# Kernel optimization log

Hardware: AMD Instinct MI355X
Metric: run time of the kernel (lower is better)

## Reference

```python
import jax, jax.numpy as jnp
import numpy as np
from jax import lax

NUM_ITER = 10
SMOOTH = 1.0
CL_WEIGHT = 0.5


def _min_pool(x, wh, ww):
    # torch: -max_pool2d(-x) pads with -inf -> min-pool with +inf boundary
    return lax.reduce_window(x, jnp.inf, lax.min,
                             (1, 1, wh, ww), (1, 1, 1, 1),
                             [(0, 0), (0, 0), (wh // 2, wh // 2), (ww // 2, ww // 2)])


def _max_pool(x, wh, ww):
    return lax.reduce_window(x, -jnp.inf, lax.max,
                             (1, 1, wh, ww), (1, 1, 1, 1),
                             [(0, 0), (0, 0), (wh // 2, wh // 2), (ww // 2, ww // 2)])


def soft_erode(img):
    return jnp.minimum(_min_pool(img, 3, 1), _min_pool(img, 1, 3))


def soft_dilate(img):
    return _max_pool(img, 3, 3)


def soft_open(img):
    return soft_dilate(soft_erode(img))


def soft_skeleton(img, num_iter=NUM_ITER):
    # img: (B,1,H,W)
    skel = jax.nn.relu(img - soft_open(img))

    def body(i, carry):
        img_e, skel = carry
        img_e = soft_erode(img_e)
        delta = jax.nn.relu(img_e - soft_open(img_e))
        skel = skel + jax.nn.relu(delta - skel * delta)
        return (img_e, skel)

    _, skel = lax.fori_loop(0, num_iter, body, (img, skel))
    return skel


def soft_dice(pred, target, smooth=SMOOTH):
    inter = jnp.sum(pred * target)
    return (2.0 * inter + smooth) / (jnp.sum(pred) + jnp.sum(target) + smooth)


def setup_inputs() -> dict:
    key = jax.random.key(0)
    k1, k2 = jax.random.split(key)
    pred = jax.random.normal(k1, (8, 1, 1024, 1024), dtype=jnp.float32)
    target = jax.random.randint(k2, (8, 1, 1024, 1024), 0, 2, dtype=jnp.int32)
    return {"pred": pred, "target": target}


def reference(pred, target):
    pred_prob = jax.nn.sigmoid(pred)          # (B,1,H,W)
    target_f = target.astype(pred_prob.dtype)

    skel_pred = soft_skeleton(pred_prob)
    skel_target = soft_skeleton(target_f)

    tprec = (jnp.sum(skel_pred * target_f) + SMOOTH) / (jnp.sum(skel_pred) + SMOOTH)
    tsens = (jnp.sum(skel_target * pred_prob) + SMOOTH) / (jnp.sum(skel_target) + SMOOTH)
    cl_dice = 2.0 * tprec * tsens / (tprec + tsens + 1e-7)

    dice = soft_dice(pred_prob, target_f)
    combined = (1.0 - CL_WEIGHT) * dice + CL_WEIGHT * cl_dice
    loss = 1.0 - combined
    return loss
```

## Files before the change

### kernel.cpp

```cpp
#include <hip/hip_runtime.h>
#include <math.h>

#define IMG  1024
#define TILE 64
#define HALO 12
#define SPP  52
#define NPRED (88*SPP)
#define SEN2 0x40004000u

typedef _Float16 h2 __attribute__((ext_vector_type(2)));
union UH { unsigned u; h2 h; };
__device__ __forceinline__ h2 u2h(unsigned u){ UH x; x.u=u; return x.h; }
__device__ __forceinline__ unsigned h2u(h2 h){ UH x; x.h=h; return x.u; }
__device__ __forceinline__ h2 pmin(h2 a, h2 b){ return __builtin_elementwise_min(a,b); }
__device__ __forceinline__ h2 pmax(h2 a, h2 b){ return __builtin_elementwise_max(a,b); }
__device__ __forceinline__ h2 funnel(h2 hi_src, h2 lo_src){
  return u2h((h2u(lo_src)>>16) | (h2u(hi_src)<<16));
}
__device__ __forceinline__ float sigmoidf(float x){ return 1.0f/(1.0f+__expf(-x)); }
__device__ __forceinline__ h2 unsent(h2 x, h2 onev, h2 zerov){
  h2 t = pmax(x-onev, zerov); return x - t - t;
}
__device__ __forceinline__ unsigned extract8(unsigned w0, unsigned w1, unsigned w2, int bp){
  unsigned long long lo = (unsigned long long)w0 | ((unsigned long long)w1<<32);
  unsigned long long hi = (unsigned long long)w1 | ((unsigned long long)w2<<32);
  unsigned a = (unsigned)(lo >> bp);
  unsigned b = (unsigned)(hi >> (bp & 31));
  return ((bp < 32) ? a : b) & 0xFFu;
}

__device__ __forceinline__ void erode2p(const unsigned* A, unsigned* B, int o){
  uint4 up = *(const uint4*)&A[o - SPP];
  uint4 c0 = *(const uint4*)&A[o];
  uint4 c1 = *(const uint4*)&A[o + SPP];
  uint4 dn = *(const uint4*)&A[o + 2*SPP];
  unsigned l0 = A[o-1], l1 = A[o+SPP-1], rr0 = A[o+4], rr1 = A[o+SPP+4];
  h2 a0=u2h(c0.x),a1=u2h(c0.y),a2=u2h(c0.z),a3=u2h(c0.w);
  h2 b0=u2h(c1.x),b1=u2h(c1.y),b2=u2h(c1.z),b3=u2h(c1.w);
  h2 va0=pmin(u2h(up.x),b0), va1=pmin(u2h(up.y),b1), va2=pmin(u2h(up.z),b2), va3=pmin(u2h(up.w),b3);
  h2 vb0=pmin(a0,u2h(dn.x)), vb1=pmin(a1,u2h(dn.y)), vb2=pmin(a2,u2h(dn.z)), vb3=pmin(a3,u2h(dn.w));
  h2 f0=funnel(a0,u2h(l0)), f1=funnel(a1,a0), f2=funnel(a2,a1), f3=funnel(a3,a2), f4=funnel(u2h(rr0),a3);
  h2 g0=funnel(b0,u2h(l1)), g1=funnel(b1,b0), g2=funnel(b2,b1), g3=funnel(b3,b2), g4=funnel(u2h(rr1),b3);
  uint4 e0,e1;
  e0.x=h2u(pmin(pmin(f0,f1),pmin(va0,a0)));
  e0.y=h2u(pmin(pmin(f1,f2),pmin(va1,a1)));
  e0.z=h2u(pmin(pmin(f2,f3),pmin(va2,a2)));
  e0.w=h2u(pmin(pmin(f3,f4),pmin(va3,a3)));
  e1.x=h2u(pmin(pmin(g0,g1),pmin(vb0,b0)));
  e1.y=h2u(pmin(pmin(g1,g2),pmin(vb1,b1)));
  e1.z=h2u(pmin(pmin(g2,g3),pmin(vb2,b2)));
  e1.w=h2u(pmin(pmin(g3,g4),pmin(vb3,b3)));
  *(uint4*)&B[o]      = e0;
  *(uint4*)&B[o+SPP]  = e1;
}

template<bool BND>
__device__ void pipeline(const float* __restrict__ pred, const int* __restrict__ targ,
                         long base, int gr0, int gc0, int tid,
                         unsigned* PA, unsigned* PB, unsigned* TAi, unsigned* TBi,
                         unsigned* sK,
                         h2 val[8], h2 skel[8], unsigned &tbits, unsigned &skbits) {
  if (!BND) {
    #pragma unroll
    for (int k=0;k<4;++k){
      int u = tid + (k<<8);
      if (u < 968) {
        int r = u/11, q = u - r*11;
        long g = base + (long)(gr0+r)*IMG + gc0 + (q<<3);
        float4 pa = *(const float4*)(pred+g);
        float4 pb = *(const float4*)(pred+g+4);
        h2 w0 = {(_Float16)sigmoidf(pa.x), (_Float16)sigmoidf(pa.y)};
        h2 w1 = {(_Float16)sigmoidf(pa.z), (_Float16)sigmoidf(pa.w)};
        h2 w2 = {(_Float16)sigmoidf(pb.x), (_Float16)sigmoidf(pb.y)};
        h2 w3 = {(_Float16)sigmoidf(pb.z), (_Float16)sigmoidf(pb.w)};
        int o = r*SPP + 2 + (q<<2);
        uint2 d0; d0.x=h2u(w0); d0.y=h2u(w1);
        uint2 d1; d1.x=h2u(w2); d1.y=h2u(w3);
        *(uint2*)&PA[o]   = d0;
        *(uint2*)&PA[o+2] = d1;
      }
    }
    #pragma unroll
    for (int k=0;k<2;++k){
      int u = tid + (k<<8);
      if (u < 264) {
        int r = u/3, w = u - r*3;
        long g = base + (long)(gr0+r)*IMG + gc0 + (w<<5);
        unsigned bits = 0;
        #pragma unroll
        for (int i=0;i<8;++i){
          if (w < 2 || i < 6) {
            int4 tv = *(const int4*)(targ + g + (i<<2));
            unsigned nib = (unsigned)(tv.x!=0) | ((unsigned)(tv.y!=0)<<1)
                         | ((unsigned)(tv.z!=0)<<2) | ((unsigned)(tv.w!=0)<<3);
            bits |= nib << (i<<2);
          }
        }
        if (w==2) bits |= 0xFF000000u;
        TAi[u] = bits;
      }
    }
  } else {
    for (int i=tid; i<88*44; i+=256){
      int r = i/44, wd = i - r*44;
      int gr = gr0 + r;
      bool rok = (unsigned)gr < (unsigned)IMG;
      int gca = gc0 + (wd<<1), gcb = gca + 1;
      _Float16 va = (_Float16)2.0f, vb = (_Float16)2.0f;
      if (rok && (unsigned)gca < (unsigned)IMG) va = (_Float16)sigmoidf(pred[base + (long)gr*IMG + gca]);
      if (rok && (unsigned)gcb < (unsigned)IMG) vb = (_Float16)sigmoidf(pred[base + (long)gr*IMG + gcb]);
      h2 w; w.x = va; w.y = vb;
      PA[r*SPP + 2 + wd] = h2u(w);
    }
    for (int u=tid; u<264; u+=256){
      int r = u/3, w = u - r*3;
      int gr = gr0 + r;
      bool rok = (unsigned)gr < (unsigned)IMG;
      unsigned bits = 0;
      for (int b=0;b<32;++b){
        int c = (w<<5) + b;
        unsigned bit = 1;
        if (c < 88) {
          int gc = gc0 + c;
          if (rok && (unsigned)gc < (unsigned)IMG) bit = (unsigned)(targ[base+(long)gr*IMG+gc] != 0);
        }
        bits |= bit << b;
      }
      TAi[u] = bits;
    }
  }
  __syncthreads();

  unsigned cm0=~0u, cm1=~0u, cm2=0x00FFFFFFu;
  bool colO = false;
  if (BND) {
    int lo = (-gc0 > 0) ? -gc0 : 0;
    int hi = (IMG - gc0 < 88) ? (IMG - gc0) : 88;
    colO = (lo > 0) || (hi < 88);
    unsigned m[3];
    #pragma unroll
    for (int w=0; w<3; ++w){
      int l = lo - (w<<5); if (l<0) l=0;
      int h = hi - (w<<5); if (h>32) h=32;
      unsigned mm = 0;
      if (h > l) {
        unsigned top = (h>=32)? ~0u : ((1u<<h)-1u);
        unsigned bot = (l<=0)? 0u : ((1u<<l)-1u);
        mm = top & ~bot;
      }
      m[w]=mm;
    }
    cm0=m[0]; cm1=m[1]; cm2=m[2] & 0x00FFFFFF;
  }

  int eo0, eo1, eo2 = 0;
  { int u=tid;     int s=u/12, q=u-s*12; eo0 = (1+(s<<1))*SPP + (q<<2); }
  { int u=tid+256; int s=u/12, q=u-s*12; eo1 = (1+(s<<1))*SPP + (q<<2); }
  const bool eex = (tid < 4);
  if (eex) { int u=tid+512; int s=u/12, q=u-s*12; eo2 = (1+(s<<1))*SPP + (q<<2); }
  const int to  = 3 + tid;
  const int twd = tid - (tid/3)*3;
  const bool tex = (tid < 2);
  const int to2  = 3 + 256 + tid;
  const int twd2 = (256+tid) - ((256+tid)/3)*3;

  const int qc = tid & 7;
  const int rg = tid >> 3;
  const int r0 = HALO + (rg<<1);
  const int wq = 8 + (qc<<2);
  const int bp = 12 + (qc<<3);

  h2 ep[8];
  {
    uint4 a0 = *(const uint4*)&PA[r0*SPP + wq];
    uint4 a1 = *(const uint4*)&PA[(r0+1)*SPP + wq];
    ep[0]=u2h(a0.x); ep[1]=u2h(a0.y); ep[2]=u2h(a0.z); ep[3]=u2h(a0.w);
    ep[4]=u2h(a1.x); ep[5]=u2h(a1.y); ep[6]=u2h(a1.z); ep[7]=u2h(a1.w);
    #pragma unroll
    for (int i=0;i<8;++i){ val[i]=ep[i]; skel[i]=(h2)(_Float16)0.0f; }
  }
  {
    int oa = r0*3, ob = (r0+1)*3;
    tbits = extract8(TAi[oa],TAi[oa+1],TAi[oa+2],bp)
          | (extract8(TAi[ob],TAi[ob+1],TAi[ob+2],bp) << 8);
  }
  unsigned tp0=0,tp1=0,tp2=0, sk0=0,sk1=0,sk2=0;
  const bool td = (tid < 64);
  const int tro = (12 + tid)*3;
  if (td) { tp0=TAi[tro]; tp1=TAi[tro+1]; tp2=TAi[tro+2]; }

  const h2 onev  = {(_Float16)1.0f,(_Float16)1.0f};
  const h2 zerov = {(_Float16)0.0f,(_Float16)0.0f};
  unsigned *A=PA, *B=PB, *Ta=TAi, *Tb=TBi;

  for (int j=0;j<11;++j){
    erode2p(A,B,eo0);
    erode2p(A,B,eo1);
    if (eex) erode2p(A,B,eo2);
    {
      unsigned own=Ta[to], up=Ta[to-3], dn=Ta[to+3];
      unsigned le = (twd>0)? Ta[to-1] : ~0u;
      unsigned ri = (twd<2)? Ta[to+1] : ~0u;
      unsigned h = own & ((own>>1)|(ri<<31)) & ((own<<1)|(le>>31));
      Tb[to] = h & up & dn;
    }
    if (tex) {
      unsigned own=Ta[to2], up=Ta[to2-3], dn=Ta[to2+3];
      unsigned le = (twd2>0)? Ta[to2-1] : ~0u;
      unsigned ri = (twd2<2)? Ta[to2+1] : ~0u;
      unsigned h = own & ((own>>1)|(ri<<31)) & ((own<<1)|(le>>31));
      Tb[to2] = h & up & dn;
    }
    __syncthreads();

    if (BND) {
      if (gr0 < 0) {
        for (int i=tid;i<12*44;i+=256){ int r=i/44; B[r*SPP+2+(i-r*44)] = SEN2; }
        if (tid < 36) Tb[tid] = ~0u;
      }
      if (gr0 + 88 > IMG) {
        for (int i=tid;i<12*44;i+=256){ int r=i/44; B[(76+r)*SPP+2+(i-r*44)] = SEN2; }
        if (tid < 36) Tb[228+tid] = ~0u;
      }
      if (colO) {
        if (gc0 < 0)
          for (int i=tid;i<88*6;i+=256){ int r=i/6; B[r*SPP+2+(i-r*6)] = SEN2; }
        if (gc0 + 88 > IMG)
          for (int i=tid;i<88*6;i+=256){ int r=i/6; B[r*SPP+40+(i-r*6)] = SEN2; }
        for (int i=tid;i<264;i+=256){
          int r=i/3, w=i-r*3;
          unsigned nm = (w==0)?~cm0:((w==1)?~cm1:~cm2);
          Tb[i] |= nm;
        }
      }
      __syncthreads();
    }

    h2 H[4][4];
    uint4 cap0, cap1;
    #pragma unroll
    for (int k=0;k<4;++k){
      int ro = (r0-1+k)*SPP + wq;
      uint4 c = *(const uint4*)&B[ro];
      h2 lw = u2h(B[ro-1]);
      h2 rw = u2h(B[ro+4]);
      if (k==1) cap0 = c;
      if (k==2) cap1 = c;
      h2 a0=u2h(c.x),a1=u2h(c.y),a2=u2h(c.z),a3=u2h(c.w);
      if (BND){
        a0=unsent(a0,onev,zerov); a1=unsent(a1,onev,zerov);
        a2=unsent(a2,onev,zerov); a3=unsent(a3,onev,zerov);
        lw=unsent(lw,onev,zerov); rw=unsent(rw,onev,zerov);
      }
      h2 f0=funnel(a0,lw), f1=funnel(a1,a0), f2=funnel(a2,a1), f3=funnel(a3,a2), f4=funnel(rw,a3);
      H[k][0]=pmax(pmax(f0,f1),a0);
      H[k][1]=pmax(pmax(f1,f2),a1);
      H[k][2]=pmax(pmax(f2,f3),a2);
      H[k][3]=pmax(pmax(f3,f4),a3);
    }
    #pragma unroll
    for (int i=0;i<4;++i){
      h2 m0 = pmax(pmax(H[0][i],H[1][i]),H[2][i]);
      h2 m1 = pmax(pmax(H[1][i],H[2][i]),H[3][i]);
      h2 d0 = pmax(ep[i]-m0, zerov);
      h2 d1 = pmax(ep[4+i]-m1, zerov);
      h2 x0 = d0 - skel[i]*d0;
      h2 x1 = d1 - skel[4+i]*d1;
      skel[i]   = skel[i]   + pmax(x0, zerov);
      skel[4+i] = skel[4+i] + pmax(x1, zerov);
    }
    ep[0]=u2h(cap0.x); ep[1]=u2h(cap0.y); ep[2]=u2h(cap0.z); ep[3]=u2h(cap0.w);
    ep[4]=u2h(cap1.x); ep[5]=u2h(cap1.y); ep[6]=u2h(cap1.z); ep[7]=u2h(cap1.w);

    if (td) {
      unsigned o0=Tb[tro], o1=Tb[tro+1], o2=Tb[tro+2];
      unsigned u0=Tb[tro-3], u1=Tb[tro-2], u2=Tb[tro-1];
      unsigned n0=Tb[tro+3], n1=Tb[tro+4], n2=Tb[tro+5];
      unsigned v0,v1,v2;
      if (BND){
        unsigned mu = ((unsigned)(gr0 + 11 + tid) < (unsigned)IMG) ? ~0u : 0u;
        unsigned md = ((unsigned)(gr0 + 13 + tid) < (unsigned)IMG) ? ~0u : 0u;
        v0 = ((u0&mu)|o0|(n0&md)) & cm0;
        v1 = ((u1&mu)|o1|(n1&md)) & cm1;
        v2 = ((u2&mu)|o2|(n2&md)) & cm2;
      } else {
        v0 = u0|o0|n0; v1 = u1|o1|n1; v2 = u2|o2|n2;
      }
      unsigned d0 = v0 | (v0<<1) | (v0>>1) | (v1<<31);
      unsigned d1 = v1 | (v1<<1) | (v0>>31) | (v1>>1) | (v2<<31);
      unsigned d2 = v2 | (v2<<1) | (v1>>31) | (v2>>1);
      sk0 |= tp0 & ~d0;
      sk1 |= tp1 & ~d1;
      sk2 |= tp2 & ~d2;
      tp0 = o0; tp1 = o1; tp2 = o2;
    }
    unsigned* t1 = A;  A = B;  B = t1;
    unsigned* t2 = Ta; Ta = Tb; Tb = t2;
  }

  if (td){ sK[3*tid] = sk0; sK[3*tid+1] = sk1; sK[3*tid+2] = sk2; }
  __syncthreads();
  {
    int o = (r0-12)*3;
    skbits = extract8(sK[o],sK[o+1],sK[o+2],bp)
           | (extract8(sK[o+3],sK[o+4],sK[o+5],bp) << 8);
  }
}

__global__ __launch_bounds__(256,4)
void cl_dice_main(const float* __restrict__ pred, const int* __restrict__ targ,
                  float* __restrict__ ws) {
  __shared__ alignas(16) unsigned sPA[NPRED];
  __shared__ alignas(16) unsigned sPB[NPRED];
  __shared__ unsigned sTA[264], sTB[264], sK[192];
  const int tid = threadIdx.x;
  const int gr0 = blockIdx.y * TILE - HALO;
  const int gc0 = blockIdx.x * TILE - HALO;
  const long base = (long)blockIdx.z * (long)(IMG * IMG);

  h2 val[8], skel[8]; unsigned tbits, skbits;
  const bool bnd = (blockIdx.x == 0) | (blockIdx.x == gridDim.x - 1) |
                   (blockIdx.y == 0) | (blockIdx.y == gridDim.y - 1);
  if (!bnd) pipeline<false>(pred, targ, base, gr0, gc0, tid, sPA, sPB, sTA, sTB, sK, val, skel, tbits, skbits);
  else      pipeline<true >(pred, targ, base, gr0, gc0, tid, sPA, sPB, sTA, sTB, sK, val, skel, tbits, skbits);

  float s[7] = {0,0,0,0,0,0,0};
  #pragma unroll
  for (int k=0;k<8;++k){
    int bb = ((k>>2)<<3) + ((k&3)<<1);
    float p0=(float)val[k].x,  p1=(float)val[k].y;
    float a0=(float)skel[k].x, a1=(float)skel[k].y;
    float t0=(float)((tbits>>bb)&1u),    t1=(float)((tbits>>(bb+1))&1u);
    float b0=(float)((skbits>>bb)&1u),   b1=(float)((skbits>>(bb+1))&1u);
    s[0]+=a0+a1;        s[1]+=a0*t0+a1*t1;
    s[2]+=b0+b1;        s[3]+=b0*p0+b1*p1;
    s[4]+=p0*t0+p1*t1;  s[5]+=p0+p1;  s[6]+=t0+t1;
  }

  float* red = (float*)sPA;
  #pragma unroll
  for (int k=0;k<7;++k){
    float v = s[k];
    v += __shfl_down(v,32); v += __shfl_down(v,16); v += __shfl_down(v,8);
    v += __shfl_down(v,4);  v += __shfl_down(v,2);  v += __shfl_down(v,1);
    if ((tid & 63) == 0) red[(tid>>6)*8 + k] = v;
  }
  __syncthreads();
  if (tid < 7) {
    float v = red[tid] + red[8+tid] + red[16+tid] + red[24+tid];
    int blk = (blockIdx.z * gridDim.y + blockIdx.y) * gridDim.x + blockIdx.x;
    ws[blk*8 + tid] = v;
  }
}

__global__ __launch_bounds__(256)
void cl_dice_finalize(const float* __restrict__ ws, float* __restrict__ out, int nblk) {
  __shared__ float red[4][8];
  int tid = threadIdx.x;
  float acc[7] = {0,0,0,0,0,0,0};
  for (int i=tid; i<nblk; i+=256) {
    #pragma unroll
    for (int k=0;k<7;++k) acc[k] += ws[i*8 + k];
  }
  #pragma unroll
  for (int k=0;k<7;++k){
    float v = acc[k];
    v += __shfl_down(v,32); v += __shfl_down(v,16); v += __shfl_down(v,8);
    v += __shfl_down(v,4);  v += __shfl_down(v,2);  v += __shfl_down(v,1);
    if ((tid & 63) == 0) red[tid>>6][k] = v;
  }
  __syncthreads();
  if (tid == 0) {
    float t0[7];
    #pragma unroll
    for (int k=0;k<7;++k) t0[k] = red[0][k] + red[1][k] + red[2][k] + red[3][k];
    float sum_sp = t0[0], sum_spt = t0[1], sum_st = t0[2], sum_stp = t0[3];
    float inter  = t0[4], sum_p   = t0[5], sum_t  = t0[6];
    float tprec = (sum_spt + 1.0f) / (sum_sp + 1.0f);
    float tsens = (sum_stp + 1.0f) / (sum_st + 1.0f);
    float cl    = 2.0f * tprec * tsens / (tprec + tsens + 1e-7f);
    float dice  = (2.0f * inter + 1.0f) / (sum_p + sum_t + 1.0f);
    out[0] = 1.0f - 0.5f * (dice + cl);
  }
}

extern "C" void kernel_launch(void* const* d_in, const int* in_sizes, int n_in,
                              void* d_out, int out_size, void* d_ws, size_t ws_size,
                              hipStream_t stream) {
  const float* pred = (const float*)d_in[0];
  const int*   targ = (const int*)d_in[1];
  float* ws  = (float*)d_ws;
  float* out = (float*)d_out;

  const int B = in_sizes[0] / (IMG * IMG);
  dim3 grid(IMG / TILE, IMG / TILE, B);
  cl_dice_main<<<grid, 256, 0, stream>>>(pred, targ, ws);

  const int nblk = (IMG / TILE) * (IMG / TILE) * B;
  cl_dice_finalize<<<1, 256, 0, stream>>>(ws, out, nblk);
}
```

Before: 249.6 us.

## Erode in place with single shared buffer and register-blocked row strips

Replaces the ping-pong shared buffers with one buffer (plus sentinel border rows) that is eroded in place. Each thread computes a strip of 5 row-pairs in registers, a barrier follows, and then the results are written back. The erode work also shrinks by iteration as the valid region narrows. Halving LDS use allows raising launch bounds to 8 blocks per CU, which targets occupancy and reuses vertical neighbours across rows, at the cost of an extra barrier per iteration and more register pressure.

Measured after the change: 321.3 us. 1.29x slower.

```diff
diff --git a/kernel.cpp b/kernel.cpp
--- a/kernel.cpp
+++ b/kernel.cpp
@@ -5,7 +5,7 @@
 #define TILE 64
 #define HALO 12
 #define SPP  52
-#define NPRED (88*SPP)
+#define NPRED (90*SPP)
 #define SEN2 0x40004000u
 
 typedef _Float16 h2 __attribute__((ext_vector_type(2)));
@@ -29,42 +29,25 @@
   return ((bp < 32) ? a : b) & 0xFFu;
 }
 
-__device__ __forceinline__ void erode2p(const unsigned* A, unsigned* B, int o){
-  uint4 up = *(const uint4*)&A[o - SPP];
-  uint4 c0 = *(const uint4*)&A[o];
-  uint4 c1 = *(const uint4*)&A[o + SPP];
-  uint4 dn = *(const uint4*)&A[o + 2*SPP];
-  unsigned l0 = A[o-1], l1 = A[o+SPP-1], rr0 = A[o+4], rr1 = A[o+SPP+4];
-  h2 a0=u2h(c0.x),a1=u2h(c0.y),a2=u2h(c0.z),a3=u2h(c0.w);
-  h2 b0=u2h(c1.x),b1=u2h(c1.y),b2=u2h(c1.z),b3=u2h(c1.w);
-  h2 va0=pmin(u2h(up.x),b0), va1=pmin(u2h(up.y),b1), va2=pmin(u2h(up.z),b2), va3=pmin(u2h(up.w),b3);
-  h2 vb0=pmin(a0,u2h(dn.x)), vb1=pmin(a1,u2h(dn.y)), vb2=pmin(a2,u2h(dn.z)), vb3=pmin(a3,u2h(dn.w));
-  h2 f0=funnel(a0,u2h(l0)), f1=funnel(a1,a0), f2=funnel(a2,a1), f3=funnel(a3,a2), f4=funnel(u2h(rr0),a3);
-  h2 g0=funnel(b0,u2h(l1)), g1=funnel(b1,b0), g2=funnel(b2,b1), g3=funnel(b3,b2), g4=funnel(u2h(rr1),b3);
-  uint4 e0,e1;
-  e0.x=h2u(pmin(pmin(f0,f1),pmin(va0,a0)));
-  e0.y=h2u(pmin(pmin(f1,f2),pmin(va1,a1)));
-  e0.z=h2u(pmin(pmin(f2,f3),pmin(va2,a2)));
-  e0.w=h2u(pmin(pmin(f3,f4),pmin(va3,a3)));
-  e1.x=h2u(pmin(pmin(g0,g1),pmin(vb0,b0)));
-  e1.y=h2u(pmin(pmin(g1,g2),pmin(vb1,b1)));
-  e1.z=h2u(pmin(pmin(g2,g3),pmin(vb2,b2)));
-  e1.w=h2u(pmin(pmin(g3,g4),pmin(vb3,b3)));
-  *(uint4*)&B[o]      = e0;
-  *(uint4*)&B[o+SPP]  = e1;
-}
-
 template<bool BND>
 __device__ void pipeline(const float* __restrict__ pred, const int* __restrict__ targ,
                          long base, int gr0, int gc0, int tid,
-                         unsigned* PA, unsigned* PB, unsigned* TAi, unsigned* TBi,
-                         unsigned* sK,
+                         unsigned* P, unsigned* Ta,
                          h2 val[8], h2 skel[8], unsigned &tbits, unsigned &skbits) {
+  for (int i = tid; i < 104; i += 256) {
+    int r = (i < 52) ? 0 : 89, c = (i < 52) ? i : i - 52;
+    P[r*SPP + c] = SEN2;
+  }
+  for (int i = tid; i < 704; i += 256) {
+    int r = 1 + (i >> 3), w = i & 7;
+    w = (w < 2) ? w : 44 + w;
+    P[r*SPP + w] = SEN2;
+  }
   if (!BND) {
     #pragma unroll
     for (int k=0;k<4;++k){
       int u = tid + (k<<8);
-      if (u < 968) {
+      if (u < 968){
         int r = u/11, q = u - r*11;
         long g = base + (long)(gr0+r)*IMG + gc0 + (q<<3);
         float4 pa = *(const float4*)(pred+g);
@@ -73,17 +56,17 @@
         h2 w1 = {(_Float16)sigmoidf(pa.z), (_Float16)sigmoidf(pa.w)};
         h2 w2 = {(_Float16)sigmoidf(pb.x), (_Float16)sigmoidf(pb.y)};
         h2 w3 = {(_Float16)sigmoidf(pb.z), (_Float16)sigmoidf(pb.w)};
-        int o = r*SPP + 2 + (q<<2);
+        int o = (1+r)*SPP + 2 + (q<<2);
         uint2 d0; d0.x=h2u(w0); d0.y=h2u(w1);
         uint2 d1; d1.x=h2u(w2); d1.y=h2u(w3);
-        *(uint2*)&PA[o]   = d0;
-        *(uint2*)&PA[o+2] = d1;
+        *(uint2*)&P[o]   = d0;
+        *(uint2*)&P[o+2] = d1;
       }
     }
     #pragma unroll
     for (int k=0;k<2;++k){
       int u = tid + (k<<8);
-      if (u < 264) {
+      if (u < 264){
         int r = u/3, w = u - r*3;
         long g = base + (long)(gr0+r)*IMG + gc0 + (w<<5);
         unsigned bits = 0;
@@ -97,7 +80,7 @@
           }
         }
         if (w==2) bits |= 0xFF000000u;
-        TAi[u] = bits;
+        Ta[u] = bits;
       }
     }
   } else {
@@ -110,7 +93,7 @@
       if (rok && (unsigned)gca < (unsigned)IMG) va = (_Float16)sigmoidf(pred[base + (long)gr*IMG + gca]);
       if (rok && (unsigned)gcb < (unsigned)IMG) vb = (_Float16)sigmoidf(pred[base + (long)gr*IMG + gcb]);
       h2 w; w.x = va; w.y = vb;
-      PA[r*SPP + 2 + wd] = h2u(w);
+      P[(1+r)*SPP + 2 + wd] = h2u(w);
     }
     for (int u=tid; u<264; u+=256){
       int r = u/3, w = u - r*3;
@@ -126,7 +109,7 @@
         }
         bits |= bit << b;
       }
-      TAi[u] = bits;
+      Ta[u] = bits;
     }
   }
   __syncthreads();
@@ -153,15 +136,14 @@
     cm0=m[0]; cm1=m[1]; cm2=m[2] & 0x00FFFFFF;
   }
 
-  int eo0, eo1, eo2 = 0;
-  { int u=tid;     int s=u/12, q=u-s*12; eo0 = (1+(s<<1))*SPP + (q<<2); }
-  { int u=tid+256; int s=u/12, q=u-s*12; eo1 = (1+(s<<1))*SPP + (q<<2); }
-  const bool eex = (tid < 4);
-  if (eex) { int u=tid+512; int s=u/12, q=u-s*12; eo2 = (1+(s<<1))*SPP + (q<<2); }
-  const int to  = 3 + tid;
+  const bool eact0 = (tid < 216);
+  const int es = tid / 12, eq = tid - es*12;
+  const int s5 = es * 5;
+  const int ew = eq << 2;
+  const int to = 3 + tid;
   const int twd = tid - (tid/3)*3;
   const bool tex = (tid < 2);
-  const int to2  = 3 + 256 + tid;
+  const int to2 = 259 + tid;
   const int twd2 = (256+tid) - ((256+tid)/3)*3;
 
   const int qc = tid & 7;
@@ -172,8 +154,8 @@
 
   h2 ep[8];
   {
-    uint4 a0 = *(const uint4*)&PA[r0*SPP + wq];
-    uint4 a1 = *(const uint4*)&PA[(r0+1)*SPP + wq];
+    uint4 a0 = *(const uint4*)&P[(r0+1)*SPP + wq];
+    uint4 a1 = *(const uint4*)&P[(r0+2)*SPP + wq];
     ep[0]=u2h(a0.x); ep[1]=u2h(a0.y); ep[2]=u2h(a0.z); ep[3]=u2h(a0.w);
     ep[4]=u2h(a1.x); ep[5]=u2h(a1.y); ep[6]=u2h(a1.z); ep[7]=u2h(a1.w);
     #pragma unroll
@@ -181,56 +163,94 @@
   }
   {
     int oa = r0*3, ob = (r0+1)*3;
-    tbits = extract8(TAi[oa],TAi[oa+1],TAi[oa+2],bp)
-          | (extract8(TAi[ob],TAi[ob+1],TAi[ob+2],bp) << 8);
+    tbits = extract8(Ta[oa],Ta[oa+1],Ta[oa+2],bp)
+          | (extract8(Ta[ob],Ta[ob+1],Ta[ob+2],bp) << 8);
   }
   unsigned tp0=0,tp1=0,tp2=0, sk0=0,sk1=0,sk2=0;
   const bool td = (tid < 64);
   const int tro = (12 + tid)*3;
-  if (td) { tp0=TAi[tro]; tp1=TAi[tro+1]; tp2=TAi[tro+2]; }
+  if (td) { tp0=Ta[tro]; tp1=Ta[tro+1]; tp2=Ta[tro+2]; }
 
   const h2 onev  = {(_Float16)1.0f,(_Float16)1.0f};
   const h2 zerov = {(_Float16)0.0f,(_Float16)0.0f};
-  unsigned *A=PA, *B=PB, *Ta=TAi, *Tb=TBi;
 
   for (int j=0;j<11;++j){
-    erode2p(A,B,eo0);
-    erode2p(A,B,eo1);
-    if (eex) erode2p(A,B,eo2);
+    uint4 e[5];
+    const bool act = eact0 && (s5+4 >= j+1) && (s5 <= 86-j);
+    if (act){
+      uint4 rw[7];
+      #pragma unroll
+      for (int t=0;t<7;++t){
+        int pr = s5 - 1 + t; pr = (pr > 88) ? 88 : pr;
+        rw[t] = *(const uint4*)&P[(pr+1)*SPP + ew];
+      }
+      h2 lw[5], rv[5];
+      #pragma unroll
+      for (int t=0;t<5;++t){
+        int pr = s5 + t; pr = (pr > 88) ? 88 : pr;
+        lw[t] = u2h(P[(pr+1)*SPP + ew - 1]);
+        rv[t] = u2h(P[(pr+1)*SPP + ew + 4]);
+      }
+      #pragma unroll
+      for (int t=0;t<5;++t){
+        h2 a0=u2h(rw[t+1].x), a1=u2h(rw[t+1].y), a2=u2h(rw[t+1].z), a3=u2h(rw[t+1].w);
+        h2 v0=pmin(u2h(rw[t].x), u2h(rw[t+2].x));
+        h2 v1=pmin(u2h(rw[t].y), u2h(rw[t+2].y));
+        h2 v2=pmin(u2h(rw[t].z), u2h(rw[t+2].z));
+        h2 v3=pmin(u2h(rw[t].w), u2h(rw[t+2].w));
+        h2 f0=funnel(a0,lw[t]), f1=funnel(a1,a0), f2=funnel(a2,a1),
+           f3=funnel(a3,a2), f4=funnel(rv[t],a3);
+        e[t].x=h2u(pmin(pmin(f0,f1),pmin(v0,a0)));
+        e[t].y=h2u(pmin(pmin(f1,f2),pmin(v1,a1)));
+        e[t].z=h2u(pmin(pmin(f2,f3),pmin(v2,a2)));
+        e[t].w=h2u(pmin(pmin(f3,f4),pmin(v3,a3)));
+      }
+    }
+    unsigned tres, tres2;
     {
       unsigned own=Ta[to], up=Ta[to-3], dn=Ta[to+3];
       unsigned le = (twd>0)? Ta[to-1] : ~0u;
       unsigned ri = (twd<2)? Ta[to+1] : ~0u;
       unsigned h = own & ((own>>1)|(ri<<31)) & ((own<<1)|(le>>31));
-      Tb[to] = h & up & dn;
-    }
-    if (tex) {
+      tres = h & up & dn;
+    }
+    if (tex){
       unsigned own=Ta[to2], up=Ta[to2-3], dn=Ta[to2+3];
       unsigned le = (twd2>0)? Ta[to2-1] : ~0u;
       unsigned ri = (twd2<2)? Ta[to2+1] : ~0u;
       unsigned h = own & ((own>>1)|(ri<<31)) & ((own<<1)|(le>>31));
-      Tb[to2] = h & up & dn;
-    }
+      tres2 = h & up & dn;
+    }
+    __syncthreads();
+    if (act){
+      #pragma unroll
+      for (int t=0;t<5;++t){
+        int pr = s5 + t; pr = (pr > 88) ? 88 : pr;
+        *(uint4*)&P[(pr+1)*SPP + ew] = e[t];
+      }
+    }
+    Ta[to] = tres;
+    if (tex) Ta[to2] = tres2;
     __syncthreads();
 
     if (BND) {
       if (gr0 < 0) {
-        for (int i=tid;i<12*44;i+=256){ int r=i/44; B[r*SPP+2+(i-r*44)] = SEN2; }
-        if (tid < 36) Tb[tid] = ~0u;
+        for (int i=tid;i<12*44;i+=256){ int r=i/44; P[(1+r)*SPP+2+(i-r*44)] = SEN2; }
+        if (tid < 36) Ta[tid] = ~0u;
       }
       if (gr0 + 88 > IMG) {
-        for (int i=tid;i<12*44;i+=256){ int r=i/44; B[(76+r)*SPP+2+(i-r*44)] = SEN2; }
-        if (tid < 36) Tb[228+tid] = ~0u;
+        for (int i=tid;i<12*44;i+=256){ int r=i/44; P[(77+r)*SPP+2+(i-r*44)] = SEN2; }
+        if (tid < 36) Ta[228+tid] = ~0u;
       }
       if (colO) {
         if (gc0 < 0)
-          for (int i=tid;i<88*6;i+=256){ int r=i/6; B[r*SPP+2+(i-r*6)] = SEN2; }
+          for (int i=tid;i<88*6;i+=256){ int r=i/6; P[(1+r)*SPP+2+(i-r*6)] = SEN2; }
         if (gc0 + 88 > IMG)
-          for (int i=tid;i<88*6;i+=256){ int r=i/6; B[r*SPP+40+(i-r*6)] = SEN2; }
+          for (int i=tid;i<88*6;i+=256){ int r=i/6; P[(1+r)*SPP+40+(i-r*6)] = SEN2; }
         for (int i=tid;i<264;i+=256){
           int r=i/3, w=i-r*3;
           unsigned nm = (w==0)?~cm0:((w==1)?~cm1:~cm2);
-          Tb[i] |= nm;
+          Ta[i] |= nm;
         }
       }
       __syncthreads();
@@ -240,19 +260,19 @@
     uint4 cap0, cap1;
     #pragma unroll
     for (int k=0;k<4;++k){
-      int ro = (r0-1+k)*SPP + wq;
-      uint4 c = *(const uint4*)&B[ro];
-      h2 lw = u2h(B[ro-1]);
-      h2 rw = u2h(B[ro+4]);
+      int ro = (r0+k)*SPP + wq;
+      uint4 c = *(const uint4*)&P[ro];
+      h2 lwv = u2h(P[ro-1]);
+      h2 rwv = u2h(P[ro+4]);
       if (k==1) cap0 = c;
       if (k==2) cap1 = c;
       h2 a0=u2h(c.x),a1=u2h(c.y),a2=u2h(c.z),a3=u2h(c.w);
       if (BND){
         a0=unsent(a0,onev,zerov); a1=unsent(a1,onev,zerov);
         a2=unsent(a2,onev,zerov); a3=unsent(a3,onev,zerov);
-        lw=unsent(lw,onev,zerov); rw=unsent(rw,onev,zerov);
-      }
-      h2 f0=funnel(a0,lw), f1=funnel(a1,a0), f2=funnel(a2,a1), f3=funnel(a3,a2), f4=funnel(rw,a3);
+        lwv=unsent(lwv,onev,zerov); rwv=unsent(rwv,onev,zerov);
+      }
+      h2 f0=funnel(a0,lwv), f1=funnel(a1,a0), f2=funnel(a2,a1), f3=funnel(a3,a2), f4=funnel(rwv,a3);
       H[k][0]=pmax(pmax(f0,f1),a0);
       H[k][1]=pmax(pmax(f1,f2),a1);
       H[k][2]=pmax(pmax(f2,f3),a2);
@@ -273,9 +293,9 @@
     ep[4]=u2h(cap1.x); ep[5]=u2h(cap1.y); ep[6]=u2h(cap1.z); ep[7]=u2h(cap1.w);
 
     if (td) {
-      unsigned o0=Tb[tro], o1=Tb[tro+1], o2=Tb[tro+2];
-      unsigned u0=Tb[tro-3], u1=Tb[tro-2], u2=Tb[tro-1];
-      unsigned n0=Tb[tro+3], n1=Tb[tro+4], n2=Tb[tro+5];
+      unsigned o0=Ta[tro], o1=Ta[tro+1], o2=Ta[tro+2];
+      unsigned u0=Ta[tro-3], u1=Ta[tro-2], u2=Ta[tro-1];
+      unsigned n0=Ta[tro+3], n1=Ta[tro+4], n2=Ta[tro+5];
       unsigned v0,v1,v2;
       if (BND){
         unsigned mu = ((unsigned)(gr0 + 11 + tid) < (unsigned)IMG) ? ~0u : 0u;
@@ -294,25 +314,23 @@
       sk2 |= tp2 & ~d2;
       tp0 = o0; tp1 = o1; tp2 = o2;
     }
-    unsigned* t1 = A;  A = B;  B = t1;
-    unsigned* t2 = Ta; Ta = Tb; Tb = t2;
-  }
-
-  if (td){ sK[3*tid] = sk0; sK[3*tid+1] = sk1; sK[3*tid+2] = sk2; }
+  }
+
+  __syncthreads();
+  if (td){ Ta[3*tid]=sk0; Ta[3*tid+1]=sk1; Ta[3*tid+2]=sk2; }
   __syncthreads();
   {
     int o = (r0-12)*3;
-    skbits = extract8(sK[o],sK[o+1],sK[o+2],bp)
-           | (extract8(sK[o+3],sK[o+4],sK[o+5],bp) << 8);
-  }
-}
-
-__global__ __launch_bounds__(256,4)
+    skbits = extract8(Ta[o],Ta[o+1],Ta[o+2],bp)
+           | (extract8(Ta[o+3],Ta[o+4],Ta[o+5],bp) << 8);
+  }
+}
+
+__global__ __launch_bounds__(256,8)
 void cl_dice_main(const float* __restrict__ pred, const int* __restrict__ targ,
                   float* __restrict__ ws) {
-  __shared__ alignas(16) unsigned sPA[NPRED];
-  __shared__ alignas(16) unsigned sPB[NPRED];
-  __shared__ unsigned sTA[264], sTB[264], sK[192];
+  __shared__ alignas(16) unsigned sP[NPRED];
+  __shared__ unsigned sTA[264];
   const int tid = threadIdx.x;
   const int gr0 = blockIdx.y * TILE - HALO;
   const int gc0 = blockIdx.x * TILE - HALO;
@@ -321,8 +339,8 @@
   h2 val[8], skel[8]; unsigned tbits, skbits;
   const bool bnd = (blockIdx.x == 0) | (blockIdx.x == gridDim.x - 1) |
                    (blockIdx.y == 0) | (blockIdx.y == gridDim.y - 1);
-  if (!bnd) pipeline<false>(pred, targ, base, gr0, gc0, tid, sPA, sPB, sTA, sTB, sK, val, skel, tbits, skbits);
-  else      pipeline<true >(pred, targ, base, gr0, gc0, tid, sPA, sPB, sTA, sTB, sK, val, skel, tbits, skbits);
+  if (!bnd) pipeline<false>(pred, targ, base, gr0, gc0, tid, sP, sTA, val, skel, tbits, skbits);
+  else      pipeline<true >(pred, targ, base, gr0, gc0, tid, sP, sTA, val, skel, tbits, skbits);
 
   float s[7] = {0,0,0,0,0,0,0};
   #pragma unroll
@@ -330,14 +348,14 @@
     int bb = ((k>>2)<<3) + ((k&3)<<1);
     float p0=(float)val[k].x,  p1=(float)val[k].y;
     float a0=(float)skel[k].x, a1=(float)skel[k].y;
-    float t0=(float)((tbits>>bb)&1u),    t1=(float)((tbits>>(bb+1))&1u);
-    float b0=(float)((skbits>>bb)&1u),   b1=(float)((skbits>>(bb+1))&1u);
+    float t0=(float)((tbits>>bb)&1u),  t1=(float)((tbits>>(bb+1))&1u);
+    float b0=(float)((skbits>>bb)&1u), b1=(float)((skbits>>(bb+1))&1u);
     s[0]+=a0+a1;        s[1]+=a0*t0+a1*t1;
     s[2]+=b0+b1;        s[3]+=b0*p0+b1*p1;
     s[4]+=p0*t0+p1*t1;  s[5]+=p0+p1;  s[6]+=t0+t1;
   }
 
-  float* red = (float*)sPA;
+  float* red = (float*)sP;
   #pragma unroll
   for (int k=0;k<7;++k){
     float v = s[k];
```
